# Performance work log

Measured on AMD Instinct MI355X. Metric: run time of the kernel, lower is better.

Reference implementation:

```python
import jax, jax.numpy as jnp
import numpy as np

N_SRC = 200000
N_DST = 100000
E = 1250000
D = 64
K = 4
ALPHA = 0.1      # alpha forward arg (nonzero -> attention/residual branch)
D_SQRT = 8.0     # self.d_sqrt
NORM_2 = -1.0    # norm_2 forward arg (default)


def setup_inputs() -> dict:
    key = jax.random.key(0)
    k1, k2, k3, k4, k5 = jax.random.split(key, 5)
    return {
        "feat_src": jax.random.normal(k1, (N_SRC, D), dtype=jnp.float32),
        "feat_dst": jax.random.normal(k2, (N_DST, D), dtype=jnp.float32),
        "pretrained_feature": jax.random.normal(k3, (N_DST, K, D), dtype=jnp.float32),
        "edge_src": jax.random.randint(k4, (E,), 0, N_SRC, dtype=jnp.int32),
        "edge_dst": jax.random.randint(k5, (E,), 0, N_DST, dtype=jnp.int32),
    }


def reference(feat_src, feat_dst, pretrained_feature, edge_src, edge_dst):
    n_src = feat_src.shape[0]
    n_dst = feat_dst.shape[0]
    ones = jnp.ones(edge_src.shape, dtype=feat_src.dtype)

    # forward aggregation: copy_u + sum over src->dst edges
    rst = jax.ops.segment_sum(feat_src[edge_src], edge_dst, num_segments=n_dst)  # [N_dst, D]
    deg_dst = jnp.clip(jax.ops.segment_sum(ones, edge_dst, num_segments=n_dst), 1.0)

    # att == 1: per-node scaled-dot attention of rst over K pretrained views
    scores = jnp.einsum('nd,nkd->nk', rst, pretrained_feature) / D_SQRT  # [N_dst, K]
    attn = jax.nn.softmax(scores, axis=1)
    pf_att = jnp.einsum('nk,nkd->nd', attn, pretrained_feature)          # [N_dst, D]
    rst = rst + ALPHA * jnp.tanh(pf_att)

    # degree normalization (in-degree^-1)
    rst = rst * (deg_dst ** -1.0)[:, None]

    # back aggregation: copy_u + sum over dst->src (reversed) edges
    bsrc = jax.ops.segment_sum(rst[edge_dst], edge_src, num_segments=n_src)  # [N_src, D]
    deg_src = jnp.clip(jax.ops.segment_sum(ones, edge_src, num_segments=n_src), 1.0)
    bsrc = bsrc * (deg_src ** NORM_2)[:, None]

    return (bsrc, rst)
```

## Files before the change

kernel.cpp:

```cpp
#include <hip/hip_runtime.h>

#define D 64


__global__ void hist_kernel(const int* __restrict__ es, const int* __restrict__ ed,
                            int* __restrict__ cnt_dst, int* __restrict__ cnt_src, int E) {
    int e = blockIdx.x * blockDim.x + threadIdx.x;
    if (e >= E) return;
    atomicAdd(&cnt_dst[ed[e]], 1);
    atomicAdd(&cnt_src[es[e]], 1);
}

__global__ void scan_partial(const int* __restrict__ cnt, int* __restrict__ part, int n) {
    int t = threadIdx.x;
    int base = blockIdx.x * 1024;
    int v = 0;
    #pragma unroll
    for (int k = 0; k < 4; ++k) {
        int i = base + k * 256 + t;
        if (i < n) v += cnt[i];
    }
    #pragma unroll
    for (int off = 32; off >= 1; off >>= 1) v += __shfl_down(v, off);
    __shared__ int wsum[4];
    if ((t & 63) == 0) wsum[t >> 6] = v;
    __syncthreads();
    if (t == 0) part[blockIdx.x] = wsum[0] + wsum[1] + wsum[2] + wsum[3];
}

__global__ void scan_exclusive_part(int* part, int nb) {
    __shared__ int sh[256];
    int t = threadIdx.x;
    int v = (t < nb) ? part[t] : 0;
    sh[t] = v;
    __syncthreads();
    for (int off = 1; off < 256; off <<= 1) {
        int x = (t >= off) ? sh[t - off] : 0;
        __syncthreads();
        sh[t] += x;
        __syncthreads();
    }
    if (t < nb) part[t] = sh[t] - v;
}

__global__ void scan_final(const int* __restrict__ cnt, const int* __restrict__ part,
                           int* __restrict__ ro, int* __restrict__ pos, int n) {
    int t = threadIdx.x;
    int base = blockIdx.x * 1024;
    int v[4];
    int tsum = 0;
    #pragma unroll
    for (int k = 0; k < 4; ++k) {
        int i = base + t * 4 + k;
        v[k] = (i < n) ? cnt[i] : 0;
        tsum += v[k];
    }
    __shared__ int sh[256];
    sh[t] = tsum;
    __syncthreads();
    for (int off = 1; off < 256; off <<= 1) {
        int x = (t >= off) ? sh[t - off] : 0;
        __syncthreads();
        sh[t] += x;
        __syncthreads();
    }
    int acc = sh[t] - tsum + part[blockIdx.x];
    #pragma unroll
    for (int k = 0; k < 4; ++k) {
        int i = base + t * 4 + k;
        if (i < n) {
            ro[i] = acc;
            pos[i] = acc;
            if (i == n - 1) ro[n] = acc + v[k];
            acc += v[k];
        }
    }
}

__global__ void fill_kernel(const int* __restrict__ es, const int* __restrict__ ed,
                            int* __restrict__ pos_dst, int* __restrict__ pos_src,
                            int* __restrict__ vals_dst, int* __restrict__ vals_src, int E) {
    int e = blockIdx.x * blockDim.x + threadIdx.x;
    if (e >= E) return;
    int s = es[e], d = ed[e];
    vals_dst[atomicAdd(&pos_dst[d], 1)] = s;
    vals_src[atomicAdd(&pos_src[s], 1)] = d;
}


__global__ void fwd_gather_attn(const float* __restrict__ feat_src,
                                const float* __restrict__ pf,
                                const int* __restrict__ ro, const int* __restrict__ vals,
                                float* __restrict__ rst, int n_dst) {
    int n = blockIdx.x * 4 + (threadIdx.x >> 6);
    int lane = threadIdx.x & 63;
    if (n >= n_dst) return;
    int beg = ro[n], end = ro[n + 1];
    float acc = 0.f;
    int j = beg;
    for (; j + 4 <= end; j += 4) {
        int s0 = vals[j], s1 = vals[j + 1], s2 = vals[j + 2], s3 = vals[j + 3];
        acc += feat_src[(size_t)s0 * D + lane];
        acc += feat_src[(size_t)s1 * D + lane];
        acc += feat_src[(size_t)s2 * D + lane];
        acc += feat_src[(size_t)s3 * D + lane];
    }
    for (; j < end; ++j) acc += feat_src[(size_t)vals[j] * D + lane];

    const float* p = pf + (size_t)n * 4 * D + lane;
    float p0 = p[0], p1 = p[D], p2 = p[2 * D], p3 = p[3 * D];
    float s0 = acc * p0, s1 = acc * p1, s2 = acc * p2, s3 = acc * p3;
    #pragma unroll
    for (int off = 32; off >= 1; off >>= 1) {
        s0 += __shfl_xor(s0, off);
        s1 += __shfl_xor(s1, off);
        s2 += __shfl_xor(s2, off);
        s3 += __shfl_xor(s3, off);
    }
    s0 *= 0.125f; s1 *= 0.125f; s2 *= 0.125f; s3 *= 0.125f;
    float m = fmaxf(fmaxf(s0, s1), fmaxf(s2, s3));
    float e0 = expf(s0 - m), e1 = expf(s1 - m), e2 = expf(s2 - m), e3 = expf(s3 - m);
    float inv = 1.0f / (e0 + e1 + e2 + e3);
    float patt = (e0 * p0 + e1 * p1 + e2 * p2 + e3 * p3) * inv;
    float out = (acc + 0.1f * tanhf(patt)) / fmaxf((float)(end - beg), 1.0f);
    rst[(size_t)n * D + lane] = out;
}

__global__ void bwd_gather(const float* __restrict__ rst,
                           const int* __restrict__ ro, const int* __restrict__ vals,
                           float* __restrict__ bsrc, int n_src) {
    int n = blockIdx.x * 4 + (threadIdx.x >> 6);
    int lane = threadIdx.x & 63;
    if (n >= n_src) return;
    int beg = ro[n], end = ro[n + 1];
    float acc = 0.f;
    int j = beg;
    for (; j + 4 <= end; j += 4) {
        int d0 = vals[j], d1 = vals[j + 1], d2 = vals[j + 2], d3 = vals[j + 3];
        acc += rst[(size_t)d0 * D + lane];
        acc += rst[(size_t)d1 * D + lane];
        acc += rst[(size_t)d2 * D + lane];
        acc += rst[(size_t)d3 * D + lane];
    }
    for (; j < end; ++j) acc += rst[(size_t)vals[j] * D + lane];
    bsrc[(size_t)n * D + lane] = acc / fmaxf((float)(end - beg), 1.0f);
}

extern "C" void kernel_launch(void* const* d_in, const int* in_sizes, int n_in,
                              void* d_out, int out_size, void* d_ws, size_t ws_size,
                              hipStream_t stream) {
    const float* feat_src = (const float*)d_in[0];
    const float* pf       = (const float*)d_in[2];
    const int*   edge_src = (const int*)d_in[3];
    const int*   edge_dst = (const int*)d_in[4];

    int n_src = in_sizes[0] / D;
    int n_dst = in_sizes[1] / D;
    int E     = in_sizes[3];

    float* bsrc = (float*)d_out;
    float* rst  = (float*)d_out + (size_t)n_src * D;

    int* w = (int*)d_ws;
    int* cnt_dst  = w;  w += n_dst;
    int* cnt_src  = w;  w += n_src;
    int* ro_dst   = w;  w += n_dst + 1;
    int* ro_src   = w;  w += n_src + 1;
    int* pos_dst  = w;  w += n_dst;
    int* pos_src  = w;  w += n_src;
    int* part_d   = w;  w += 256;
    int* part_s   = w;  w += 256;
    int* vals_dst = w;  w += E;
    int* vals_src = w;  w += E;

    hipMemsetAsync(cnt_dst, 0, (size_t)(n_dst + n_src) * sizeof(int), stream);

    int nb_dst = (n_dst + 1023) / 1024;
    int nb_src = (n_src + 1023) / 1024;

    hist_kernel<<<(E + 255) / 256, 256, 0, stream>>>(edge_src, edge_dst, cnt_dst, cnt_src, E);

    scan_partial<<<nb_dst, 256, 0, stream>>>(cnt_dst, part_d, n_dst);
    scan_partial<<<nb_src, 256, 0, stream>>>(cnt_src, part_s, n_src);
    scan_exclusive_part<<<1, 256, 0, stream>>>(part_d, nb_dst);
    scan_exclusive_part<<<1, 256, 0, stream>>>(part_s, nb_src);
    scan_final<<<nb_dst, 256, 0, stream>>>(cnt_dst, part_d, ro_dst, pos_dst, n_dst);
    scan_final<<<nb_src, 256, 0, stream>>>(cnt_src, part_s, ro_src, pos_src, n_src);

    fill_kernel<<<(E + 255) / 256, 256, 0, stream>>>(edge_src, edge_dst, pos_dst, pos_src,
                                                     vals_dst, vals_src, E);

    fwd_gather_attn<<<(n_dst + 3) / 4, 256, 0, stream>>>(feat_src, pf, ro_dst, vals_dst,
                                                         rst, n_dst);
    bwd_gather<<<(n_src + 3) / 4, 256, 0, stream>>>(rst, ro_src, vals_src, bsrc, n_src);
}
```

Measured before the change: 670.2 us.

## Build CSR via two-level bucket partition instead of per-node atomics

```diff
diff --git a/kernel.cpp b/kernel.cpp
--- a/kernel.cpp
+++ b/kernel.cpp
@@ -1,92 +1,72 @@
 #include <hip/hip_runtime.h>
 
 #define D 64
+#define BSH 5
 
-
-__global__ void hist_kernel(const int* __restrict__ es, const int* __restrict__ ed,
-                            int* __restrict__ cnt_dst, int* __restrict__ cnt_src, int E) {
+__global__ void bucket_hist(const int* __restrict__ es, const int* __restrict__ ed,
+                            int* __restrict__ bcnt_d, int* __restrict__ bcnt_s, int E) {
     int e = blockIdx.x * blockDim.x + threadIdx.x;
     if (e >= E) return;
-    atomicAdd(&cnt_dst[ed[e]], 1);
-    atomicAdd(&cnt_src[es[e]], 1);
+    atomicAdd(&bcnt_d[ed[e] >> BSH], 1);
+    atomicAdd(&bcnt_s[es[e] >> BSH], 1);
 }
 
-__global__ void scan_partial(const int* __restrict__ cnt, int* __restrict__ part, int n) {
+__global__ void bucket_scan(const int* __restrict__ cnt, int* __restrict__ base,
+                            int* __restrict__ bpos, int n) {
+    const int T = 256;
     int t = threadIdx.x;
-    int base = blockIdx.x * 1024;
-    int v = 0;
-    #pragma unroll
-    for (int k = 0; k < 4; ++k) {
-        int i = base + k * 256 + t;
-        if (i < n) v += cnt[i];
-    }
-    #pragma unroll
-    for (int off = 32; off >= 1; off >>= 1) v += __shfl_down(v, off);
-    __shared__ int wsum[4];
-    if ((t & 63) == 0) wsum[t >> 6] = v;
+    int C = (n + T - 1) / T;
+    int lo = t * C, hi = min(lo + C, n);
+    int s = 0;
+    for (int i = lo; i < hi; ++i) s += cnt[i];
+    __shared__ int sh[T];
+    sh[t] = s;
     __syncthreads();
-    if (t == 0) part[blockIdx.x] = wsum[0] + wsum[1] + wsum[2] + wsum[3];
-}
-
-__global__ void scan_exclusive_part(int* part, int nb) {
-    __shared__ int sh[256];
-    int t = threadIdx.x;
-    int v = (t < nb) ? part[t] : 0;
-    sh[t] = v;
-    __syncthreads();
-    for (int off = 1; off < 256; off <<= 1) {
+    for (int off = 1; off < T; off <<= 1) {
         int x = (t >= off) ? sh[t - off] : 0;
         __syncthreads();
         sh[t] += x;
         __syncthreads();
     }
-    if (t < nb) part[t] = sh[t] - v;
+    int a = sh[t] - s;
+    for (int i = lo; i < hi; ++i) { int c = cnt[i]; base[i] = a; bpos[i] = a; a += c; }
+    if (t == T - 1) base[n] = sh[T - 1];
 }
 
-__global__ void scan_final(const int* __restrict__ cnt, const int* __restrict__ part,
-                           int* __restrict__ ro, int* __restrict__ pos, int n) {
-    int t = threadIdx.x;
-    int base = blockIdx.x * 1024;
-    int v[4];
-    int tsum = 0;
-    #pragma unroll
-    for (int k = 0; k < 4; ++k) {
-        int i = base + t * 4 + k;
-        v[k] = (i < n) ? cnt[i] : 0;
-        tsum += v[k];
-    }
-    __shared__ int sh[256];
-    sh[t] = tsum;
-    __syncthreads();
-    for (int off = 1; off < 256; off <<= 1) {
-        int x = (t >= off) ? sh[t - off] : 0;
-        __syncthreads();
-        sh[t] += x;
-        __syncthreads();
-    }
-    int acc = sh[t] - tsum + part[blockIdx.x];
-    #pragma unroll
-    for (int k = 0; k < 4; ++k) {
-        int i = base + t * 4 + k;
-        if (i < n) {
-            ro[i] = acc;
-            pos[i] = acc;
-            if (i == n - 1) ro[n] = acc + v[k];
-            acc += v[k];
-        }
-    }
-}
-
-__global__ void fill_kernel(const int* __restrict__ es, const int* __restrict__ ed,
-                            int* __restrict__ pos_dst, int* __restrict__ pos_src,
-                            int* __restrict__ vals_dst, int* __restrict__ vals_src, int E) {
+__global__ void partition(const int* __restrict__ es, const int* __restrict__ ed,
+                          int2* __restrict__ pd, int2* __restrict__ ps,
+                          int* __restrict__ bpos_d, int* __restrict__ bpos_s, int E) {
     int e = blockIdx.x * blockDim.x + threadIdx.x;
     if (e >= E) return;
     int s = es[e], d = ed[e];
-    vals_dst[atomicAdd(&pos_dst[d], 1)] = s;
-    vals_src[atomicAdd(&pos_src[s], 1)] = d;
+    pd[atomicAdd(&bpos_d[d >> BSH], 1)] = make_int2(s, d);
+    ps[atomicAdd(&bpos_s[s >> BSH], 1)] = make_int2(d, s);
 }
 
+__global__ void finalize(const int2* __restrict__ pairs, const int* __restrict__ bbase,
+                         int* __restrict__ ro, int* __restrict__ vals, int n, int nb) {
+    int b = blockIdx.x;
+    int t = threadIdx.x;
+    if (b >= nb) return;
+    int beg = bbase[b], end = bbase[b + 1];
+    __shared__ int cnt[32], pos[32], sc[33];
+    if (t < 32) { cnt[t] = 0; pos[t] = 0; }
+    __syncthreads();
+    for (int j = beg + t; j < end; j += blockDim.x)
+        atomicAdd(&cnt[pairs[j].y & 31], 1);
+    __syncthreads();
+    if (t == 0) { int a = 0; for (int i = 0; i < 32; ++i) { sc[i] = a; a += cnt[i]; } sc[32] = a; }
+    __syncthreads();
+    int node0 = b << BSH;
+    if (t < 32 && node0 + t < n) ro[node0 + t] = beg + sc[t];
+    if (b == nb - 1 && t == 0) ro[n] = end;
+    for (int j = beg + t; j < end; j += blockDim.x) {
+        int2 pr = pairs[j];
+        int ln = pr.y & 31;
+        int p = atomicAdd(&pos[ln], 1);
+        vals[beg + sc[ln] + p] = pr.x;
+    }
+}
 
 __global__ void fwd_gather_attn(const float* __restrict__ feat_src,
                                 const float* __restrict__ pf,
@@ -158,39 +138,37 @@
     int n_dst = in_sizes[1] / D;
     int E     = in_sizes[3];
 
+    int nb_d = (n_dst + 31) >> BSH;
+    int nb_s = (n_src + 31) >> BSH;
+
     float* bsrc = (float*)d_out;
     float* rst  = (float*)d_out + (size_t)n_src * D;
 
+    int2* pairs_d = (int2*)d_out;
+    int2* pairs_s = pairs_d + E;
+
     int* w = (int*)d_ws;
-    int* cnt_dst  = w;  w += n_dst;
-    int* cnt_src  = w;  w += n_src;
-    int* ro_dst   = w;  w += n_dst + 1;
-    int* ro_src   = w;  w += n_src + 1;
-    int* pos_dst  = w;  w += n_dst;
-    int* pos_src  = w;  w += n_src;
-    int* part_d   = w;  w += 256;
-    int* part_s   = w;  w += 256;
-    int* vals_dst = w;  w += E;
-    int* vals_src = w;  w += E;
+    int* bcnt_d  = w;  w += nb_d;
+    int* bcnt_s  = w;  w += nb_s;
+    int* bbase_d = w;  w += nb_d + 1;
+    int* bbase_s = w;  w += nb_s + 1;
+    int* bpos_d  = w;  w += nb_d;
+    int* bpos_s  = w;  w += nb_s;
+    int* ro_d    = w;  w += n_dst + 1;
+    int* ro_s    = w;  w += n_src + 1;
+    int* vals_d  = w;  w += E;
+    int* vals_s  = w;  w += E;
 
-    hipMemsetAsync(cnt_dst, 0, (size_t)(n_dst + n_src) * sizeof(int), stream);
+    hipMemsetAsync(bcnt_d, 0, (size_t)(nb_d + nb_s) * sizeof(int), stream);
 
-    int nb_dst = (n_dst + 1023) / 1024;
-    int nb_src = (n_src + 1023) / 1024;
+    bucket_hist<<<(E + 255) / 256, 256, 0, stream>>>(edge_src, edge_dst, bcnt_d, bcnt_s, E);
+    bucket_scan<<<1, 256, 0, stream>>>(bcnt_d, bbase_d, bpos_d, nb_d);
+    bucket_scan<<<1, 256, 0, stream>>>(bcnt_s, bbase_s, bpos_s, nb_s);
+    partition<<<(E + 255) / 256, 256, 0, stream>>>(edge_src, edge_dst, pairs_d, pairs_s,
+                                                   bpos_d, bpos_s, E);
+    finalize<<<nb_d, 256, 0, stream>>>(pairs_d, bbase_d, ro_d, vals_d, n_dst, nb_d);
+    finalize<<<nb_s, 256, 0, stream>>>(pairs_s, bbase_s, ro_s, vals_s, n_src, nb_s);
 
-    hist_kernel<<<(E + 255) / 256, 256, 0, stream>>>(edge_src, edge_dst, cnt_dst, cnt_src, E);
-
-    scan_partial<<<nb_dst, 256, 0, stream>>>(cnt_dst, part_d, n_dst);
-    scan_partial<<<nb_src, 256, 0, stream>>>(cnt_src, part_s, n_src);
-    scan_exclusive_part<<<1, 256, 0, stream>>>(part_d, nb_dst);
-    scan_exclusive_part<<<1, 256, 0, stream>>>(part_s, nb_src);
-    scan_final<<<nb_dst, 256, 0, stream>>>(cnt_dst, part_d, ro_dst, pos_dst, n_dst);
-    scan_final<<<nb_src, 256, 0, stream>>>(cnt_src, part_s, ro_src, pos_src, n_src);
-
-    fill_kernel<<<(E + 255) / 256, 256, 0, stream>>>(edge_src, edge_dst, pos_dst, pos_src,
-                                                     vals_dst, vals_src, E);
-
-    fwd_gather_attn<<<(n_dst + 3) / 4, 256, 0, stream>>>(feat_src, pf, ro_dst, vals_dst,
-                                                         rst, n_dst);
-    bwd_gather<<<(n_src + 3) / 4, 256, 0, stream>>>(rst, ro_src, vals_src, bsrc, n_src);
+    fwd_gather_attn<<<(n_dst + 3) / 4, 256, 0, stream>>>(feat_src, pf, ro_d, vals_d, rst, n_dst);
+    bwd_gather<<<(n_src + 3) / 4, 256, 0, stream>>>(rst, ro_s, vals_s, bsrc, n_src);
 }
```

After: 705.5 us. 1.05x slower.
